# Kernel optimization log

Measured on AMD Instinct MI355X. Metric: run time of the kernel, lower is better.

The kernel has to match this reference:

```python
import jax, jax.numpy as jnp
import numpy as np
from jax import lax

B, N, T = 64, 50, 30          # batch, history length, words per title
VOCAB, E = 50000, 300          # vocab size, word emb dim
FN, A, G, K = 400, 200, 400, 3 # filter_num, attention_dim, gru_unit, window size
USERS = 50000


def setup_inputs() -> dict:
    key = jax.random.key(0)
    ks = jax.random.split(key, 12)
    return {
        "user_id": jax.random.randint(ks[0], (B,), 0, USERS),
        "history_title": jax.random.randint(ks[1], (B, N, T), 0, VOCAB),
        "history_length": jax.random.randint(ks[2], (B,), 1, N + 1),
        "word_emb": jax.random.normal(ks[3], (VOCAB, E), jnp.float32) * 0.02,
        "conv_w": jax.random.normal(ks[4], (K, E, FN), jnp.float32) * 0.05,  # WIO layout
        "conv_b": jnp.zeros((FN,), jnp.float32),
        "v": jax.random.normal(ks[5], (FN, A), jnp.float32) * 0.05,
        "vb": jnp.zeros((A,), jnp.float32),
        "q": jax.random.normal(ks[6], (A, 1), jnp.float32) * 0.05,
        "user_emb": jax.random.normal(ks[7], (USERS, G), jnp.float32) * 0.02,
        "W_ih": jax.random.normal(ks[8], (3 * G, FN), jnp.float32) * 0.05,
        "W_hh": jax.random.normal(ks[9], (3 * G, G), jnp.float32) * 0.05,
        "b_ih": jnp.zeros((3 * G,), jnp.float32),
        "b_hh": jnp.zeros((3 * G,), jnp.float32),
    }


def _news_encode(history_title, word_emb, conv_w, conv_b, v, vb, q):
    # word embedding lookup: [B, N, T, E] (dropout is identity in eval mode)
    W = word_emb[history_title]
    # Conv1d over the word axis, padding=1 keeps length T
    x = W.reshape(B * N, T, E)
    C = lax.conv_general_dilated(
        x, conv_w, window_strides=(1,), padding=[(1, 1)],
        dimension_numbers=("NWC", "WIO", "NWC")) + conv_b
    C = jax.nn.relu(C).reshape(B, N, T, FN)
    # additive attention scores
    a = jnp.tanh(jnp.einsum("bntf,fa->bnta", C, v) + vb)
    a = jnp.einsum("bnta,ao->bnt", a, q)  # q: [A,1] -> squeeze
    # original uses Softmax(dim=0) on a [n, t] per sample => over the n-titles axis
    alpha = jax.nn.softmax(a, axis=1)
    # e[i] = alpha[i] @ C[i]: weighted sum over words -> [B, N, FN]
    return jnp.einsum("bnt,bntf->bnf", alpha, C)


def _gru(news_embed, h0, lengths, W_ih, W_hh, b_ih, b_hh):
    # packed_padded semantics: h stops updating once step >= length
    xs = jnp.swapaxes(news_embed, 0, 1)                 # [N, B, FN]
    mask = jnp.arange(N)[:, None] < lengths[None, :]    # [N, B]

    def step(h, inp):
        x_t, m = inp
        gx = x_t @ W_ih.T + b_ih                        # [B, 3G]
        gh = h @ W_hh.T + b_hh
        xr, xz, xn = jnp.split(gx, 3, axis=-1)
        hr, hz, hn = jnp.split(gh, 3, axis=-1)
        r = jax.nn.sigmoid(xr + hr)
        z = jax.nn.sigmoid(xz + hz)
        n = jnp.tanh(xn + r * hn)
        h_new = (1.0 - z) * n + z * h
        h = jnp.where(m[:, None], h_new, h)
        return h, None

    h_final, _ = lax.scan(step, h0, (xs, mask))
    return h_final


def reference(user_id, history_title, history_length, word_emb, conv_w, conv_b,
              v, vb, q, user_emb, W_ih, W_hh, b_ih, b_hh):
    news_embed = _news_encode(history_title, word_emb, conv_w, conv_b, v, vb, q)
    h0 = user_emb[user_id]                              # [B, G]
    return _gru(news_embed, h0, history_length, W_ih, W_hh, b_ih, b_hh)
```

## Files before the change

kernel.cpp:

```cpp
#include <hip/hip_runtime.h>
#include <hip/hip_bf16.h>

#define BB 64
#define NN 50
#define TT 30
#define EE 300
#define FN 400
#define AA 200
#define GG 400

typedef __attribute__((ext_vector_type(8))) short bf16x8;
typedef __attribute__((ext_vector_type(4))) float f32x4;

__device__ inline ushort f2bf(float x) {
  __hip_bfloat16 b = __float2bfloat16(x);
  return *(ushort*)&b;
}

__global__ void k_prep_all(
    const float* __restrict__ Whh, const float* __restrict__ cw,
    const float* __restrict__ v, const float* __restrict__ q,
    const float* __restrict__ vb, const float* __restrict__ Wih,
    const int* __restrict__ user_id, const float* __restrict__ user_emb,
    float* __restrict__ Wpack, __hip_bfloat16* __restrict__ WT2,
    __hip_bfloat16* __restrict__ vT2, float* __restrict__ qp,
    float* __restrict__ vbp, __hip_bfloat16* __restrict__ Wih_bf,
    float* __restrict__ h0)
{
  int i = blockIdx.x * 256 + threadIdx.x;
  if (i < 480000) {
    int jl = i % 150;
    int g = (i / 150) % 400;
    int gc = i / 60000;
    int gate = jl / 50, gl = jl - gate * 50;
    int j = gate * 400 + gc * 50 + gl;
    Wpack[i] = Whh[j * 400 + g];
  } else if (i < 910080) {
    int k = i - 480000;
    int kk = k & 31, f = (k >> 5) % 448, s = k / (448 * 32);
    int ko = s / 10, e = (s - ko * 10) * 32 + kk;
    float val = (f < FN && e < EE) ? cw[(ko * EE + e) * FN + f] : 0.f;
    WT2[k] = __float2bfloat16(val);
  } else if (i < 1003264) {
    int k = i - 910080;
    int kk = k & 31, a = (k >> 5) % 224, ks = k / (224 * 32);
    int e = ks * 32 + kk;
    float val = (a < AA && e < FN) ? v[e * AA + a] : 0.f;
    vT2[k] = __float2bfloat16(val);
  } else if (i < 1003488) {
    int k = i - 1003264;
    qp[k]  = k < AA ? q[k]  : 0.f;
    vbp[k] = k < AA ? vb[k] : 0.f;
  } else if (i < 1562592) {
    int k = i - 1003488;
    int j = k / 416, f = k % 416;
    Wih_bf[k] = __float2bfloat16((j < 1200 && f < FN) ? Wih[j * 400 + f] : 0.f);
  } else if (i < 1588192) {
    int k = i - 1562592;
    int b = k / GG, g = k - b * GG;
    h0[k] = user_emb[(size_t)user_id[b] * GG + g];
  }
}

__global__ void k_prep_emb(const float* __restrict__ w, __hip_bfloat16* __restrict__ o) {
  int i = blockIdx.x * 256 + threadIdx.x;
  if (i < 50000 * 80) {
    int row = i / 80, cg = i - row * 80;
    ushort4 u4 = make_ushort4(0, 0, 0, 0);
    if (cg < 75) {
      float4 v4 = *(const float4*)(w + (size_t)row * EE + cg * 4);
      u4 = make_ushort4(f2bf(v4.x), f2bf(v4.y), f2bf(v4.z), f2bf(v4.w));
    }
    *(ushort4*)((ushort*)o + (size_t)row * 320 + cg * 4) = u4;
  }
}

__global__ __launch_bounds__(256, 2) void k_conv(
    const int* __restrict__ title, const __hip_bfloat16* __restrict__ emb,
    const __hip_bfloat16* __restrict__ WT2, const float* __restrict__ conv_b,
    __hip_bfloat16* __restrict__ C)
{
  __shared__ __align__(16) ushort E[2][34][344];
  __shared__ int words[60];
  const int g = blockIdx.x;
  const int tid = threadIdx.x;
  const int lane = tid & 63, wn = tid >> 6;
  const int l15 = lane & 15, l4 = lane >> 4;

  if (tid < 60) words[tid] = title[g * 60 + tid];
  for (int idx = tid; idx < 2924; idx += 256)
    *(uint4*)((ushort*)E + idx * 8) = make_uint4(0u, 0u, 0u, 0u);
  __syncthreads();
  for (int idx = tid; idx < 2400; idx += 256) {
    int row = idx / 40, c = idx - row * 40;
    int tt = row / 30, w = row - tt * 30;
    *(uint4*)(&E[tt][w + 1][c * 8]) =
        *(const uint4*)((const ushort*)emb + (size_t)words[row] * 320 + c * 8);
  }
  __syncthreads();

  f32x4 acc[4][7];
#pragma unroll
  for (int nt = 0; nt < 7; ++nt) {
    int f = wn * 112 + nt * 16 + l15;
    float bj = (f < FN) ? conv_b[f] : 0.f;
#pragma unroll
    for (int mt = 0; mt < 4; ++mt) {
      acc[mt][nt][0] = bj; acc[mt][nt][1] = bj;
      acc[mt][nt][2] = bj; acc[mt][nt][3] = bj;
    }
  }

  const ushort* Bbase = (const ushort*)WT2 + (size_t)(wn * 112 + l15) * 32 + l4 * 8;

#define LOADB(dst, s) {                                                        \
    const ushort* p_ = Bbase + (size_t)(s) * 14336;                            \
    _Pragma("unroll")                                                          \
    for (int nt = 0; nt < 7; ++nt) dst[nt] = *(const bf16x8*)(p_ + nt * 512);  \
  }
#define DOMFMA(bq, s) {                                                        \
    const int ko_ = (s) / 10, ks_ = (s) % 10;                                  \
    bf16x8 af_[4];                                                             \
    _Pragma("unroll")                                                          \
    for (int mt = 0; mt < 4; ++mt)                                             \
      af_[mt] = *(const bf16x8*)(&E[mt >> 1][(mt & 1) * 16 + l15 + ko_]        \
                                   [ks_ * 32 + l4 * 8]);                       \
    _Pragma("unroll")                                                          \
    for (int nt = 0; nt < 7; ++nt)                                             \
      _Pragma("unroll")                                                        \
      for (int mt = 0; mt < 4; ++mt)                                           \
        acc[mt][nt] = __builtin_amdgcn_mfma_f32_16x16x32_bf16(                 \
            af_[mt], bq[nt], acc[mt][nt], 0, 0, 0);                            \
  }

  bf16x8 bqA[7], bqB[7];
  LOADB(bqA, 0);
#pragma unroll
  for (int it = 0; it < 15; ++it) {
    const int s0 = it * 2;
    LOADB(bqB, s0 + 1);
    DOMFMA(bqA, s0);
    if (it < 14) LOADB(bqA, s0 + 2);
    DOMFMA(bqB, s0 + 1);
  }
#undef LOADB
#undef DOMFMA

#pragma unroll
  for (int mt = 0; mt < 4; ++mt) {
    const int ti = mt >> 1;
    const int tb = (mt & 1) * 16 + l4 * 4;
#pragma unroll
    for (int nt = 0; nt < 7; ++nt) {
      int f = wn * 112 + nt * 16 + l15;
      if (f < 416) {
#pragma unroll
        for (int r = 0; r < 4; ++r) {
          int t = tb + r;
          if (t < TT) {
            ushort us = f2bf(fmaxf(acc[mt][nt][r], 0.f));
            __builtin_nontemporal_store(
                us, (ushort*)C + ((size_t)(g * 2 + ti) * 30 + t) * 416 + f);
          }
        }
      }
    }
  }
}

__global__ __launch_bounds__(512) void k_attn(
    const __hip_bfloat16* __restrict__ C, const __hip_bfloat16* __restrict__ vT2,
    const float* __restrict__ vbp, const float* __restrict__ qp,
    float* __restrict__ score)
{
  __shared__ float sred[2][256];
  const int tid = threadIdx.x;
  const int lane = tid & 63, wid = tid >> 6;
  const int wm = wid >> 1, wn = wid & 1;
  const int l15 = lane & 15, l4 = lane >> 4;
  const size_t row0 = (size_t)blockIdx.x * 256;

  f32x4 acc[4][7];
  float ql[7];
#pragma unroll
  for (int nt = 0; nt < 7; ++nt) {
    int a = wn * 112 + nt * 16 + l15;
    ql[nt] = qp[a];
    float vbv = vbp[a];
#pragma unroll
    for (int mt = 0; mt < 4; ++mt) {
      acc[mt][nt][0] = vbv; acc[mt][nt][1] = vbv;
      acc[mt][nt][2] = vbv; acc[mt][nt][3] = vbv;
    }
  }

  const ushort* Vbase = (const ushort*)vT2 + (size_t)(wn * 112 + l15) * 32 + l4 * 8;
  const ushort* Cbase = (const ushort*)C + (row0 + wm * 64 + l15) * 416 + l4 * 8;

  for (int ks = 0; ks < 13; ++ks) {
    bf16x8 vf[7];
#pragma unroll
    for (int nt = 0; nt < 7; ++nt)
      vf[nt] = *(const bf16x8*)(Vbase + ((size_t)ks * 224 + nt * 16) * 32);
    bf16x8 cf[4];
#pragma unroll
    for (int mt = 0; mt < 4; ++mt)
      cf[mt] = __builtin_nontemporal_load(
          (const bf16x8*)(Cbase + (size_t)mt * 16 * 416 + ks * 32));
#pragma unroll
    for (int nt = 0; nt < 7; ++nt)
#pragma unroll
      for (int mt = 0; mt < 4; ++mt)
        acc[mt][nt] = __builtin_amdgcn_mfma_f32_16x16x32_bf16(cf[mt], vf[nt], acc[mt][nt], 0, 0, 0);
  }

  float sums[4][4];
#pragma unroll
  for (int mt = 0; mt < 4; ++mt)
#pragma unroll
    for (int r = 0; r < 4; ++r) sums[mt][r] = 0.f;
#pragma unroll
  for (int mt = 0; mt < 4; ++mt)
#pragma unroll
    for (int nt = 0; nt < 7; ++nt)
#pragma unroll
      for (int r = 0; r < 4; ++r)
        sums[mt][r] += tanhf(acc[mt][nt][r]) * ql[nt];
#pragma unroll
  for (int mask = 1; mask < 16; mask <<= 1)
#pragma unroll
    for (int mt = 0; mt < 4; ++mt)
#pragma unroll
      for (int r = 0; r < 4; ++r)
        sums[mt][r] += __shfl_xor(sums[mt][r], mask);

  float outv = 0.f;
#pragma unroll
  for (int mt = 0; mt < 4; ++mt)
#pragma unroll
    for (int r = 0; r < 4; ++r)
      if (l15 == mt * 4 + r) outv = sums[mt][r];
  sred[wn][wm * 64 + (l15 >> 2) * 16 + l4 * 4 + (l15 & 3)] = outv;
  __syncthreads();
  if (tid < 256) score[row0 + tid] = sred[0][tid] + sred[1][tid];
}

__global__ void k2_softmax_n(const float* __restrict__ score, float* __restrict__ alpha) {
  int i = blockIdx.x * 256 + threadIdx.x;
  if (i >= BB * TT) return;
  int b = i / TT, t = i - b * TT;
  int base = b * (NN * TT) + t;
  float m = -1e30f;
  for (int n = 0; n < NN; ++n) m = fmaxf(m, score[base + n * TT]);
  float s = 0.f;
  for (int n = 0; n < NN; ++n) s += __expf(score[base + n * TT] - m);
  float inv = 1.f / s;
  for (int n = 0; n < NN; ++n)
    alpha[base + n * TT] = __expf(score[base + n * TT] - m) * inv;
}

__global__ __launch_bounds__(256) void k3_wsum(
    const float* __restrict__ alpha, const __hip_bfloat16* __restrict__ C,
    __hip_bfloat16* __restrict__ Ebf) {
  __shared__ float al[TT];
  const int bn = blockIdx.x;
  const int tid = threadIdx.x;
  if (tid < TT) al[tid] = alpha[bn * TT + tid];
  __syncthreads();
  for (int f = tid; f < 416; f += 256) {
    float s = 0.f;
    if (f < FN) {
#pragma unroll
      for (int t = 0; t < TT; ++t)
        s = fmaf(al[t], __bfloat162float(C[((size_t)bn * TT + t) * 416 + f]), s);
    }
    Ebf[(size_t)bn * 416 + f] = __float2bfloat16(s);
  }
}

__global__ __launch_bounds__(512) void k4_gx_mfma(
    const __hip_bfloat16* __restrict__ Ebf,
    const __hip_bfloat16* __restrict__ Wih,
    const float* __restrict__ b_ih,
    float* __restrict__ gx)
{
  __shared__ __align__(16) ushort Alds[128 * 40];
  __shared__ __align__(16) ushort Blds[448 * 40];
  const int tid = threadIdx.x;
  const int lane = tid & 63, wid = tid >> 6;
  const int wm = wid >> 2, wn = wid & 3;
  const int l15 = lane & 15, l4 = lane >> 4;
  const int mb = blockIdx.x / 3;
  const int nb = blockIdx.x - mb * 3;
  const int row0 = mb * 128;
  const int n0 = nb * 448;

  f32x4 acc[4][7];
#pragma unroll
  for (int nt = 0; nt < 7; ++nt) {
    int j = n0 + wn * 112 + nt * 16 + l15;
    float bj = (j < 1200) ? b_ih[j] : 0.f;
#pragma unroll
    for (int mt = 0; mt < 4; ++mt) {
      acc[mt][nt][0] = bj; acc[mt][nt][1] = bj;
      acc[mt][nt][2] = bj; acc[mt][nt][3] = bj;
    }
  }

  const int ar = tid >> 2, ac = tid & 3;
  for (int ks = 0; ks < 13; ++ks) {
    *(uint4*)(&Alds[ar * 40 + ac * 8]) =
        *(const uint4*)((const ushort*)Ebf + (size_t)(row0 + ar) * 416 + ks * 32 + ac * 8);
    for (int idx = tid; idx < 1792; idx += 512) {
      int r = idx >> 2, c = idx & 3;
      *(uint4*)(&Blds[r * 40 + c * 8]) =
          *(const uint4*)((const ushort*)Wih + (size_t)(n0 + r) * 416 + ks * 32 + c * 8);
    }
    __syncthreads();
    bf16x8 af[4];
#pragma unroll
    for (int mt = 0; mt < 4; ++mt)
      af[mt] = *(const bf16x8*)(&Alds[(wm * 64 + mt * 16 + l15) * 40 + l4 * 8]);
#pragma unroll
    for (int nt = 0; nt < 7; ++nt) {
      bf16x8 bfr = *(const bf16x8*)(&Blds[(wn * 112 + nt * 16 + l15) * 40 + l4 * 8]);
#pragma unroll
      for (int mt = 0; mt < 4; ++mt)
        acc[mt][nt] = __builtin_amdgcn_mfma_f32_16x16x32_bf16(af[mt], bfr, acc[mt][nt], 0, 0, 0);
    }
    __syncthreads();
  }

#pragma unroll
  for (int mt = 0; mt < 4; ++mt) {
    int row = row0 + wm * 64 + mt * 16 + l4 * 4;
#pragma unroll
    for (int nt = 0; nt < 7; ++nt) {
      int j = n0 + wn * 112 + nt * 16 + l15;
      if (j < 1200) {
#pragma unroll
        for (int r = 0; r < 4; ++r)
          gx[(size_t)(row + r) * 1200 + j] = acc[mt][nt][r];
      }
    }
  }
}

__global__ __launch_bounds__(256) void k5_step(
    const float* __restrict__ h_prev, float* __restrict__ h_next,
    const float* __restrict__ Wpack, const float* __restrict__ b_hh,
    const float* __restrict__ gx, const int* __restrict__ hist_len,
    float* __restrict__ out, int step)
{
  const int gc = blockIdx.x & 7;
  const int bg = blockIdx.x >> 3;
  const int tid = threadIdx.x;
  __shared__ float ghl[2][3][50];

  if (tid < 150) {
    const float* h0p = h_prev + (size_t)(2 * bg) * GG;
    const float* h1p = h0p + GG;
    float a00 = 0.f, a01 = 0.f, a10 = 0.f, a11 = 0.f;
    const float* wp = Wpack + (size_t)gc * 60000 + tid;
#pragma unroll 8
    for (int g = 0; g < 200; ++g) {
      float w0 = wp[g * 150];
      float w1 = wp[(g + 200) * 150];
      float h00 = h0p[g], h01 = h0p[g + 200];
      float h10 = h1p[g], h11 = h1p[g + 200];
      a00 = fmaf(h00, w0, a00);
      a10 = fmaf(h10, w0, a10);
      a01 = fmaf(h01, w1, a01);
      a11 = fmaf(h11, w1, a11);
    }
    int gate = tid / 50, gl = tid - gate * 50;
    float bb = b_hh[gate * 400 + gc * 50 + gl];
    ghl[0][gate][gl] = a00 + a01 + bb;
    ghl[1][gate][gl] = a10 + a11 + bb;
  }
  __syncthreads();

  if (tid < 100) {
    int b = tid / 50, gl = tid - (tid / 50) * 50;
    int babs = 2 * bg + b;
    int g = gc * 50 + gl;
    const float* gxp = gx + ((size_t)babs * NN + step) * 1200;
    float xr = gxp[g], xz = gxp[400 + g], xn = gxp[800 + g];
    float hr = ghl[b][0][gl], hz = ghl[b][1][gl], hn = ghl[b][2][gl];
    float r = 1.f / (1.f + __expf(-(xr + hr)));
    float z = 1.f / (1.f + __expf(-(xz + hz)));
    float nv = tanhf(xn + r * hn);
    float hold = h_prev[(size_t)babs * GG + g];
    float hnew = (1.f - z) * nv + z * hold;
    float hres = (step < hist_len[babs]) ? hnew : hold;
    h_next[(size_t)babs * GG + g] = hres;
    if (step == NN - 1) out[(size_t)babs * GG + g] = hres;
  }
}

extern "C" void kernel_launch(void* const* d_in, const int* in_sizes, int n_in,
                              void* d_out, int out_size, void* d_ws, size_t ws_size,
                              hipStream_t stream) {
  const int*   user_id   = (const int*)d_in[0];
  const int*   title     = (const int*)d_in[1];
  const int*   hist_len  = (const int*)d_in[2];
  const float* word_emb  = (const float*)d_in[3];
  const float* conv_w    = (const float*)d_in[4];
  const float* conv_b    = (const float*)d_in[5];
  const float* v         = (const float*)d_in[6];
  const float* vb        = (const float*)d_in[7];
  const float* q         = (const float*)d_in[8];
  const float* user_emb  = (const float*)d_in[9];
  const float* W_ih      = (const float*)d_in[10];
  const float* W_hh      = (const float*)d_in[11];
  const float* b_ih      = (const float*)d_in[12];
  const float* b_hh      = (const float*)d_in[13];
  float* out = (float*)d_out;

  char* ws = (char*)d_ws;
  size_t off = 0;
  auto take = [&](size_t bytes) {
    char* p = ws + off;
    off = (off + bytes + 255) & ~(size_t)255;
    return p;
  };
  __hip_bfloat16* C      = (__hip_bfloat16*)take((size_t)BB * NN * TT * 416 * 2);
  float* score  = (float*)take((size_t)BB * NN * TT * 4);
  float* alpha  = (float*)take((size_t)BB * NN * TT * 4);
  __hip_bfloat16* Ebf    = (__hip_bfloat16*)take((size_t)BB * NN * 416 * 2);
  __hip_bfloat16* Wih_bf = (__hip_bfloat16*)take((size_t)1344 * 416 * 2);
  float* Wpack  = (float*)take((size_t)8 * 400 * 150 * 4);
  float* gx     = (float*)take((size_t)BB * NN * 1200 * 4);
  float* h0     = (float*)take((size_t)BB * GG * 4);
  float* h1     = (float*)take((size_t)BB * GG * 4);
  __hip_bfloat16* emb_bf = (__hip_bfloat16*)take((size_t)50000 * 320 * 2);
  __hip_bfloat16* WT2    = (__hip_bfloat16*)take((size_t)30 * 448 * 32 * 2);
  __hip_bfloat16* vT2    = (__hip_bfloat16*)take((size_t)13 * 224 * 32 * 2);
  float* qp     = (float*)take(224 * 4);
  float* vbp    = (float*)take(224 * 4);
  (void)ws_size;

  k_prep_all<<<6204, 256, 0, stream>>>(W_hh, conv_w, v, q, vb, W_ih, user_id,
                                       user_emb, Wpack, WT2, vT2, qp, vbp,
                                       Wih_bf, h0);
  k_prep_emb<<<(50000 * 80 + 255) / 256, 256, 0, stream>>>(word_emb, emb_bf);

  k_conv<<<BB * NN / 2, 256, 0, stream>>>(title, emb_bf, WT2, conv_b, C);
  k_attn<<<BB * NN * TT / 256, 512, 0, stream>>>(C, vT2, vbp, qp, score);
  k2_softmax_n<<<(BB * TT + 255) / 256, 256, 0, stream>>>(score, alpha);
  k3_wsum<<<BB * NN, 256, 0, stream>>>(alpha, C, Ebf);
  k4_gx_mfma<<<75, 512, 0, stream>>>(Ebf, Wih_bf, b_ih, gx);

  float* hbuf[2] = {h0, h1};
  for (int step = 0; step < NN; ++step) {
    k5_step<<<256, 256, 0, stream>>>(hbuf[step & 1], hbuf[(step + 1) & 1],
                                     Wpack, b_hh, gx, hist_len, out, step);
  }
}
```

Measured before the change: 990.9 us.

## Drop manual B-fragment double buffering and nontemporal hints in conv/attn

Replaces the hand-written double-buffered weight-fragment prefetch in the conv kernel with a plain fully unrolled loop, leaving load scheduling to the compiler. It also shrinks the LDS row pitch from 344 to 332 elements, which changes the bank-conflict pattern and the LDS footprint. The nontemporal store of C in conv and the nontemporal load of C in attention become ordinary accesses, so the intermediate can stay in cache between the two kernels. It risks losing explicit overlap of global weight loads with the MFMA work.

```diff
diff --git a/kernel.cpp b/kernel.cpp
--- a/kernel.cpp
+++ b/kernel.cpp
@@ -80,7 +80,7 @@
     const __hip_bfloat16* __restrict__ WT2, const float* __restrict__ conv_b,
     __hip_bfloat16* __restrict__ C)
 {
-  __shared__ __align__(16) ushort E[2][34][344];
+  __shared__ __align__(16) ushort E[2][34][332];
   __shared__ int words[60];
   const int g = blockIdx.x;
   const int tid = threadIdx.x;
@@ -88,7 +88,7 @@
   const int l15 = lane & 15, l4 = lane >> 4;
 
   if (tid < 60) words[tid] = title[g * 60 + tid];
-  for (int idx = tid; idx < 2924; idx += 256)
+  for (int idx = tid; idx < 2822; idx += 256)
     *(uint4*)((ushort*)E + idx * 8) = make_uint4(0u, 0u, 0u, 0u);
   __syncthreads();
   for (int idx = tid; idx < 2400; idx += 256) {
@@ -113,38 +113,26 @@
 
   const ushort* Bbase = (const ushort*)WT2 + (size_t)(wn * 112 + l15) * 32 + l4 * 8;
 
-#define LOADB(dst, s) {                                                        \
-    const ushort* p_ = Bbase + (size_t)(s) * 14336;                            \
-    _Pragma("unroll")                                                          \
-    for (int nt = 0; nt < 7; ++nt) dst[nt] = *(const bf16x8*)(p_ + nt * 512);  \
-  }
-#define DOMFMA(bq, s) {                                                        \
-    const int ko_ = (s) / 10, ks_ = (s) % 10;                                  \
-    bf16x8 af_[4];                                                             \
-    _Pragma("unroll")                                                          \
-    for (int mt = 0; mt < 4; ++mt)                                             \
-      af_[mt] = *(const bf16x8*)(&E[mt >> 1][(mt & 1) * 16 + l15 + ko_]        \
-                                   [ks_ * 32 + l4 * 8]);                       \
-    _Pragma("unroll")                                                          \
-    for (int nt = 0; nt < 7; ++nt)                                             \
-      _Pragma("unroll")                                                        \
-      for (int mt = 0; mt < 4; ++mt)                                           \
-        acc[mt][nt] = __builtin_amdgcn_mfma_f32_16x16x32_bf16(                 \
-            af_[mt], bq[nt], acc[mt][nt], 0, 0, 0);                            \
-  }
-
-  bf16x8 bqA[7], bqB[7];
-  LOADB(bqA, 0);
-#pragma unroll
-  for (int it = 0; it < 15; ++it) {
-    const int s0 = it * 2;
-    LOADB(bqB, s0 + 1);
-    DOMFMA(bqA, s0);
-    if (it < 14) LOADB(bqA, s0 + 2);
-    DOMFMA(bqB, s0 + 1);
-  }
-#undef LOADB
-#undef DOMFMA
+#pragma unroll
+  for (int ko = 0; ko < 3; ++ko) {
+#pragma unroll
+    for (int ks = 0; ks < 10; ++ks) {
+      const int s = ko * 10 + ks;
+      bf16x8 bq[7];
+#pragma unroll
+      for (int nt = 0; nt < 7; ++nt)
+        bq[nt] = *(const bf16x8*)(Bbase + (size_t)s * 14336 + nt * 512);
+      bf16x8 af[4];
+#pragma unroll
+      for (int mt = 0; mt < 4; ++mt)
+        af[mt] = *(const bf16x8*)(&E[mt >> 1][(mt & 1) * 16 + l15 + ko][ks * 32 + l4 * 8]);
+#pragma unroll
+      for (int nt = 0; nt < 7; ++nt)
+#pragma unroll
+        for (int mt = 0; mt < 4; ++mt)
+          acc[mt][nt] = __builtin_amdgcn_mfma_f32_16x16x32_bf16(af[mt], bq[nt], acc[mt][nt], 0, 0, 0);
+    }
+  }
 
 #pragma unroll
   for (int mt = 0; mt < 4; ++mt) {
@@ -158,9 +146,8 @@
         for (int r = 0; r < 4; ++r) {
           int t = tb + r;
           if (t < TT) {
-            ushort us = f2bf(fmaxf(acc[mt][nt][r], 0.f));
-            __builtin_nontemporal_store(
-                us, (ushort*)C + ((size_t)(g * 2 + ti) * 30 + t) * 416 + f);
+            float vv = fmaxf(acc[mt][nt][r], 0.f);
+            C[((size_t)(g * 2 + ti) * 30 + t) * 416 + f] = __float2bfloat16(vv);
           }
         }
       }
@@ -205,8 +192,7 @@
     bf16x8 cf[4];
 #pragma unroll
     for (int mt = 0; mt < 4; ++mt)
-      cf[mt] = __builtin_nontemporal_load(
-          (const bf16x8*)(Cbase + (size_t)mt * 16 * 416 + ks * 32));
+      cf[mt] = *(const bf16x8*)(Cbase + (size_t)mt * 16 * 416 + ks * 32);
 #pragma unroll
     for (int nt = 0; nt < 7; ++nt)
 #pragma unroll
```

Measured after the change: 955.5 us. -3.6%, faster.
